# Performance work log

Hardware: AMD Instinct MI355X
Metric: run time of the kernel (lower is better)

## Reference

```python
import jax, jax.numpy as jnp
import numpy as np

B, T, H, W = 2, 16, 16, 16
C_IN, C_ORIG, N_RES, KC, VC = 256, 3, 4, 16, 128
C_ATT = C_IN + C_ORIG          # 259, used for 1/sqrt(c) scale
C_PE = C_ATT + 3               # 262, conv input channels after pos-enc concat
NEG = jnp.float32(-1e30)


def setup_inputs() -> dict:
    key = jax.random.key(0)
    ks = jax.random.split(key, 12)
    f32 = jnp.float32

    def wt(k, shape, fan_in):
        return (jax.random.normal(k, shape, dtype=f32) / np.float32(np.sqrt(fan_in)))

    return {
        "x": jax.random.normal(ks[0], (B, C_IN, T, H, W), dtype=f32),
        "original_input": jax.random.normal(ks[1], (B, C_ORIG, T, H, W), dtype=f32),
        # residual blocks (stacked over N_RES): kernel-2 conv3d, padding 1
        "rb_w1": wt(ks[2], (N_RES, C_IN, C_IN, 2, 2, 2), C_IN * 8),
        "rb_b1": jnp.zeros((N_RES, C_IN), f32),
        "rb_w2": wt(ks[3], (N_RES, 2 * C_IN, C_IN, 2, 2, 2), C_IN * 8),
        "rb_b2": jnp.zeros((N_RES, 2 * C_IN), f32),
        # attention q/k/v 1x1 conv3d == per-pixel linear on 262 channels
        "q_w": wt(ks[4], (KC, C_PE), C_PE), "q_b": jnp.zeros((KC,), f32),
        "k_w": wt(ks[5], (KC, C_PE), C_PE), "k_b": jnp.zeros((KC,), f32),
        "v_w": wt(ks[6], (VC, C_PE), C_PE), "v_b": jnp.zeros((VC,), f32),
        # attention_conv (1x1), res_conv (1x1), out_conv (1x1)
        "attn_w": wt(ks[7], (C_IN, VC), VC), "attn_b": jnp.zeros((C_IN,), f32),
        "resc_w": wt(ks[8], (C_IN, C_IN), C_IN), "resc_b": jnp.zeros((C_IN,), f32),
        "out_w": wt(ks[9], (C_IN, C_IN), C_IN), "out_b": jnp.zeros((C_IN,), f32),
    }


def _conv3d(x, w, b, pad):
    y = jax.lax.conv_general_dilated(
        x, w, window_strides=(1, 1, 1), padding=[(pad, pad)] * 3,
        dimension_numbers=("NCDHW", "OIDHW", "NCDHW"))
    return y + b[None, :, None, None, None]


def _c1(x, w, b):  # 1x1x1 conv
    return jnp.einsum("bcthw,oc->bothw", x, w) + b[None, :, None, None, None]


def _pos_enc(b, t, h, w):
    zt = (-0.5 + jnp.arange(t, dtype=jnp.float32) / t)[None, None, :, None, None]
    zh = (-0.5 + jnp.arange(h, dtype=jnp.float32) / h)[None, None, None, :, None]
    zw = (-0.5 + jnp.arange(w, dtype=jnp.float32) / w)[None, None, None, None, :]
    shp = (b, 1, t, h, w)
    return jnp.concatenate([jnp.broadcast_to(zt, shp),
                            jnp.broadcast_to(zh, shp),
                            jnp.broadcast_to(zw, shp)], axis=1)


def _forward(x, original_input, rb_w1, rb_b1, rb_w2, rb_b2,
             q_w, q_b, k_w, k_b, v_w, v_b,
             attn_w, attn_b, resc_w, resc_b, out_w, out_b):
    b, _, t, h, w = x.shape
    elu = jax.nn.elu

    # --- residual blocks (attention=True variant: k=2 convs, pad=1, crop) ---
    res = x
    for i in range(N_RES):
        o = elu(_conv3d(elu(res), rb_w1[i], rb_b1[i], 1))[:, :, :t, :h, :w]
        o = _conv3d(o, rb_w2[i], rb_b2[i], 1)[:, :, :t, :h, :w]
        c2 = o.shape[1] // 2
        res = res + o[:, :c2] * jax.nn.sigmoid(o[:, c2:])  # gated (identity act)

    # --- attention block on concat(res, original_input) + pos-enc ---
    xa = jnp.concatenate([res, original_input], axis=1)          # (b,259,t,h,w)
    xa = jnp.concatenate([xa, _pos_enc(b, t, h, w)], axis=1)     # (b,262,t,h,w)
    seq = t * h * w
    xf = xa.reshape(b, C_PE, seq).transpose(0, 2, 1)             # (b,seq,262)
    q = xf @ q_w.T + q_b
    k = xf @ k_w.T + k_b
    v = xf @ v_w.T + v_b                                         # (b,seq,VC)

    scores = jnp.einsum("bqc,bkc->bqk", q, k) / np.float32(np.sqrt(C_ATT))
    mask = jnp.tril(jnp.ones((seq, seq), dtype=bool), k=-1)      # mask_center=True
    p = jax.nn.softmax(jnp.where(mask, scores, NEG), axis=-1)
    p = jnp.where(mask, p, 0.0)                                  # row 0 -> zeros
    att = jnp.einsum("bqk,bkc->bqc", p, v)                       # (b,seq,VC)
    att = att.transpose(0, 2, 1).reshape(b, VC, t, h, w)

    att = elu(_c1(elu(att), attn_w, attn_b))
    res = elu(_c1(elu(res), resc_w, resc_b))
    return elu(_c1(elu(res + att), out_w, out_b))


def reference(x, original_input, rb_w1, rb_b1, rb_w2, rb_b2,
              q_w, q_b, k_w, k_b, v_w, v_b,
              attn_w, attn_b, resc_w, resc_b, out_w, out_b):
    return _forward(x, original_input, rb_w1, rb_b1, rb_w2, rb_b2,
                    q_w, q_b, k_w, k_b, v_w, v_b,
                    attn_w, attn_b, resc_w, resc_b, out_w, out_b)
```

## Files before the change

kernel.cpp:

```cpp
#include <hip/hip_runtime.h>
#include <math.h>

#define SEQ 4096
#define CIN 256
#define PROWS 4913
#define PT 289
#define LROW 40
#define NROWS 170
#define GROW 36

typedef __attribute__((ext_vector_type(8))) short bf16x8;
typedef __attribute__((ext_vector_type(4))) float f32x4;

__device__ __forceinline__ float elu_f(float x) {
    return x > 0.0f ? x : (expf(x) - 1.0f);
}
__device__ __forceinline__ unsigned short f2b(float f) {
    unsigned int u = __float_as_uint(f);
    return (unsigned short)((u + 0x7FFFu + ((u >> 16) & 1u)) >> 16);
}

__global__ __launch_bounds__(256) void zero2_kernel(
    uint4* __restrict__ p1, uint4* __restrict__ p2, int n)
{
    int i = blockIdx.x * 256 + threadIdx.x;
    if (i < n) {
        p1[i] = (uint4){0, 0, 0, 0};
        p2[i] = (uint4){0, 0, 0, 0};
    }
}

__global__ __launch_bounds__(256) void prep_t(
    const float* __restrict__ x, unsigned short* __restrict__ elub)
{
    const int b = blockIdx.x >> 5;
    const int s0 = (blockIdx.x & 31) << 7;
    const int cg = blockIdx.y;
    const int tid = threadIdx.x;
    const int s = s0 + (tid & 127);
    const int c0 = cg * 32 + (tid >> 7) * 16;
    const int tt = s >> 8, hh = (s >> 4) & 15, ww = s & 15;
    const size_t prow = (size_t)b * PROWS + (tt + 1) * PT + (hh + 1) * 17 + (ww + 1);
    unsigned short ev[16];
#pragma unroll
    for (int cc = 0; cc < 16; ++cc) {
        float v = x[(((size_t)(b * 256 + c0 + cc)) << 12) + s];
        ev[cc] = f2b(elu_f(v));
    }
    unsigned short* ep = &elub[prow * 256 + c0];
    *(ushort4*)(ep)      = *(ushort4*)&ev[0];
    *(ushort4*)(ep + 4)  = *(ushort4*)&ev[4];
    *(ushort4*)(ep + 8)  = *(ushort4*)&ev[8];
    *(ushort4*)(ep + 12) = *(ushort4*)&ev[12];
}

__global__ __launch_bounds__(256) void wcvt_kernel(
    const float* __restrict__ w1, const float* __restrict__ w2,
    unsigned short* __restrict__ w1t, unsigned short* __restrict__ w2t)
{
    int idx = blockIdx.x * 256 + threadIdx.x;
    if (idx < 2097152) {
        int layer = idx >> 19;
        int rem = idx & 0x7FFFF;
        int frag = rem >> 9;
        int l = (rem >> 3) & 63;
        int e = rem & 7;
        int ks = frag >> 4, mt = frag & 15;
        int tap = ks >> 3, kc = ks & 7;
        int co = mt * 16 + (l & 15);
        int ci = kc * 32 + (l >> 4) * 8 + e;
        w1t[idx] = f2b(w1[(((size_t)(layer * 256 + co)) * 256 + ci) * 8 + tap]);
    }
    if (idx < 4194304) {
        int layer = idx >> 20;
        int rem = idx & 0xFFFFF;
        int frag = rem >> 9;
        int l = (rem >> 3) & 63;
        int e = rem & 7;
        int ks = frag >> 5, mt = frag & 31;
        int tap = ks >> 3, kc = ks & 7;
        int rp = mt * 16 + (l & 15);
        int grp = rp >> 5, sub = rp & 31;
        int co = (sub < 16) ? (grp * 16 + sub) : (256 + grp * 16 + (sub - 16));
        int ci = kc * 32 + (l >> 4) * 8 + e;
        w2t[idx] = f2b(w2[(((size_t)(layer * 512 + co)) * 256 + ci) * 8 + tap]);
    }
}

__global__ __launch_bounds__(256) void conv1_mfma(
    const unsigned short* __restrict__ inP,
    const unsigned short* __restrict__ wfrag,
    const float* __restrict__ bias,
    unsigned short* __restrict__ outP)
{
    __shared__ unsigned short sX[NROWS * LROW];

    const int bx = blockIdx.x;
    const int b = bx >> 6, ptile = bx & 63;
    const int t = ptile >> 2, h0 = (ptile & 3) << 2;
    const int mt0 = blockIdx.y << 2;
    const int tid = threadIdx.x;
    const int lane = tid & 63, wv = tid >> 6;
    const int lr = lane & 15, lg = lane >> 4;

    const unsigned short* inB = inP + (size_t)b * PROWS * 256;

    f32x4 acc[4];
#pragma unroll
    for (int mi = 0; mi < 4; ++mi) acc[mi] = (f32x4){0.f, 0.f, 0.f, 0.f};

    for (int kc = 0; kc < 8; ++kc) {
        const int ci0 = kc << 5;
        __syncthreads();
#pragma unroll
        for (int rnd = 0; rnd < 3; ++rnd) {
            int task = tid + (rnd << 8);
            int row = task >> 2, q = task & 3;
            if (row < NROWS) {
                int dt = row / 85, rem = row - dt * 85;
                int dh = rem / 17, dw = rem - dh * 17;
                int prow = (t + dt) * PT + (h0 + dh) * 17 + dw;
                *(bf16x8*)&sX[row * LROW + (q << 3)] =
                    *(const bf16x8*)(inB + (size_t)prow * 256 + ci0 + (q << 3));
            }
        }
        __syncthreads();
#pragma unroll
        for (int tap = 0; tap < 8; ++tap) {
            const unsigned short* wp = wfrag +
                ((size_t)((((tap << 3) + kc) << 4) + mt0) << 9) + (lane << 3);
            bf16x8 a0 = *(const bf16x8*)(wp);
            bf16x8 a1 = *(const bf16x8*)(wp + 512);
            bf16x8 a2 = *(const bf16x8*)(wp + 1024);
            bf16x8 a3 = *(const bf16x8*)(wp + 1536);
            const int rb = (tap >> 2) * 85 + (wv + ((tap >> 1) & 1)) * 17 + (tap & 1);
            bf16x8 xb = *(const bf16x8*)&sX[(rb + lr) * LROW + (lg << 3)];
            acc[0] = __builtin_amdgcn_mfma_f32_16x16x32_bf16(a0, xb, acc[0], 0, 0, 0);
            acc[1] = __builtin_amdgcn_mfma_f32_16x16x32_bf16(a1, xb, acc[1], 0, 0, 0);
            acc[2] = __builtin_amdgcn_mfma_f32_16x16x32_bf16(a2, xb, acc[2], 0, 0, 0);
            acc[3] = __builtin_amdgcn_mfma_f32_16x16x32_bf16(a3, xb, acc[3], 0, 0, 0);
        }
    }
    const size_t orow = (size_t)b * PROWS + (t + 1) * PT + (h0 + wv + 1) * 17 + (lr + 1);
#pragma unroll
    for (int mi = 0; mi < 4; ++mi) {
        const int cob = ((mt0 + mi) << 4) + (lg << 2);
        unsigned short v4[4];
#pragma unroll
        for (int r = 0; r < 4; ++r)
            v4[r] = f2b(elu_f(acc[mi][r] + bias[cob + r]));
        *(ushort4*)&outP[orow * 256 + cob] = *(ushort4*)v4;
    }
}

__global__ __launch_bounds__(256) void conv2_mfma(
    const unsigned short* __restrict__ inP,
    const unsigned short* __restrict__ wfrag,
    const float* __restrict__ bias,
    float* __restrict__ resf,
    unsigned short* __restrict__ elub)
{
    __shared__ unsigned short sX[NROWS * LROW];

    const int bx = blockIdx.x;
    const int b = bx >> 6, ptile = bx & 63;
    const int t = ptile >> 2, h0 = (ptile & 3) << 2;
    const int mt0 = blockIdx.y << 2;
    const int tid = threadIdx.x;
    const int lane = tid & 63, wv = tid >> 6;
    const int lr = lane & 15, lg = lane >> 4;

    const unsigned short* inB = inP + (size_t)b * PROWS * 256;

    f32x4 acc[4];
#pragma unroll
    for (int mi = 0; mi < 4; ++mi) acc[mi] = (f32x4){0.f, 0.f, 0.f, 0.f};

    for (int kc = 0; kc < 8; ++kc) {
        const int ci0 = kc << 5;
        __syncthreads();
#pragma unroll
        for (int rnd = 0; rnd < 3; ++rnd) {
            int task = tid + (rnd << 8);
            int row = task >> 2, q = task & 3;
            if (row < NROWS) {
                int dt = row / 85, rem = row - dt * 85;
                int dh = rem / 17, dw = rem - dh * 17;
                int prow = (t + dt) * PT + (h0 + dh) * 17 + dw;
                *(bf16x8*)&sX[row * LROW + (q << 3)] =
                    *(const bf16x8*)(inB + (size_t)prow * 256 + ci0 + (q << 3));
            }
        }
        __syncthreads();
#pragma unroll
        for (int tap = 0; tap < 8; ++tap) {
            const unsigned short* wp = wfrag +
                ((size_t)((((tap << 3) + kc) << 5) + mt0) << 9) + (lane << 3);
            bf16x8 a0 = *(const bf16x8*)(wp);
            bf16x8 a1 = *(const bf16x8*)(wp + 512);
            bf16x8 a2 = *(const bf16x8*)(wp + 1024);
            bf16x8 a3 = *(const bf16x8*)(wp + 1536);
            const int rb = (tap >> 2) * 85 + (wv + ((tap >> 1) & 1)) * 17 + (tap & 1);
            bf16x8 xb = *(const bf16x8*)&sX[(rb + lr) * LROW + (lg << 3)];
            acc[0] = __builtin_amdgcn_mfma_f32_16x16x32_bf16(a0, xb, acc[0], 0, 0, 0);
            acc[1] = __builtin_amdgcn_mfma_f32_16x16x32_bf16(a1, xb, acc[1], 0, 0, 0);
            acc[2] = __builtin_amdgcn_mfma_f32_16x16x32_bf16(a2, xb, acc[2], 0, 0, 0);
            acc[3] = __builtin_amdgcn_mfma_f32_16x16x32_bf16(a3, xb, acc[3], 0, 0, 0);
        }
    }
    const int s = (t << 8) + ((h0 + wv) << 4) + lr;
    const size_t prow = (size_t)b * PROWS + (t + 1) * PT + (h0 + wv + 1) * 17 + (lr + 1);
#pragma unroll
    for (int p = 0; p < 2; ++p) {
        const int chb = (((mt0 >> 1) + p) << 4) + (lg << 2);
        unsigned short e4[4];
#pragma unroll
        for (int r = 0; r < 4; ++r) {
            const int ch = chb + r;
            float av = acc[2 * p][r] + bias[ch];
            float gv = acc[2 * p + 1][r] + bias[ch + 256];
            float add = av / (1.0f + expf(-gv));
            size_t ridx = (((size_t)(b * 256 + ch)) << 12) + s;
            float rn = resf[ridx] + add;
            resf[ridx] = rn;
            e4[r] = f2b(elu_f(rn));
        }
        *(ushort4*)&elub[prow * 256 + chb] = *(ushort4*)e4;
    }
}

__global__ __launch_bounds__(256) void pack_kernel(
    const float* __restrict__ res, const float* __restrict__ orig,
    unsigned short* __restrict__ xq)
{
    const int b = blockIdx.x >> 5;
    const int s0 = (blockIdx.x & 31) << 7;
    const int cg = blockIdx.y;
    const int tid = threadIdx.x;
    const int s = s0 + (tid & 127);
    const int c0 = cg * 32 + (tid >> 7) * 16;

    unsigned short xv[16];
    if (cg < 8) {
#pragma unroll
        for (int cc = 0; cc < 16; ++cc) {
            int c = c0 + cc;
            float v = res[(size_t)((b * 256 + c) << 12) + s];
            xv[cc] = f2b(v);
        }
    } else if (cg == 8) {
#pragma unroll
        for (int cc = 0; cc < 16; ++cc) {
            int c = c0 + cc;
            float v;
            if (c < 259)      v = orig[(size_t)((b * 3 + (c - 256)) << 12) + s];
            else if (c == 259) v = -0.5f + (float)(s >> 8) * 0.0625f;
            else if (c == 260) v = -0.5f + (float)((s >> 4) & 15) * 0.0625f;
            else if (c == 261) v = -0.5f + (float)(s & 15) * 0.0625f;
            else               v = 0.0f;
            xv[cc] = f2b(v);
        }
    } else {
#pragma unroll
        for (int cc = 0; cc < 16; ++cc) xv[cc] = 0;
    }
    unsigned short* xp = &xq[((size_t)(b << 12) + s) * 320 + c0];
    *(ushort4*)(xp)      = *(ushort4*)&xv[0];
    *(ushort4*)(xp + 4)  = *(ushort4*)&xv[4];
    *(ushort4*)(xp + 8)  = *(ushort4*)&xv[8];
    *(ushort4*)(xp + 12) = *(ushort4*)&xv[12];
}

__global__ __launch_bounds__(256) void wcvt2_kernel(
    const float* __restrict__ qw, const float* __restrict__ kw,
    const float* __restrict__ vw, const float* __restrict__ aw,
    const float* __restrict__ rw, const float* __restrict__ ow,
    unsigned short* __restrict__ wqkv, unsigned short* __restrict__ awb,
    unsigned short* __restrict__ rwb, unsigned short* __restrict__ owb)
{
    int idx = blockIdx.x * 256 + threadIdx.x;
    if (idx < 61440) {
        int frag = idx >> 9, l = (idx >> 3) & 63, e = idx & 7;
        int kc = frag / 12, mt = frag - kc * 12;
        int r = mt * 16 + (l & 15);
        int c = kc * 32 + ((l >> 4) << 3) + e;
        float v = 0.0f;
        if (c < 262) {
            if (r < 16)       v = qw[r * 262 + c];
            else if (r < 32)  v = kw[(r - 16) * 262 + c];
            else if (r < 160) v = vw[(r - 32) * 262 + c];
        }
        wqkv[idx] = f2b(v);
    } else if (idx < 94208) {
        int j = idx - 61440;
        int frag = j >> 9, l = (j >> 3) & 63, e = j & 7;
        int kc = frag >> 4, mt = frag & 15;
        int r = mt * 16 + (l & 15);
        int c = kc * 32 + ((l >> 4) << 3) + e;
        awb[j] = f2b(aw[r * 128 + c]);
    } else if (idx < 159744) {
        int j = idx - 94208;
        int frag = j >> 9, l = (j >> 3) & 63, e = j & 7;
        int kc = frag >> 4, mt = frag & 15;
        int r = mt * 16 + (l & 15);
        int c = kc * 32 + ((l >> 4) << 3) + e;
        rwb[j] = f2b(rw[r * 256 + c]);
    } else if (idx < 225280) {
        int j = idx - 159744;
        int frag = j >> 9, l = (j >> 3) & 63, e = j & 7;
        int kc = frag >> 4, mt = frag & 15;
        int r = mt * 16 + (l & 15);
        int c = kc * 32 + ((l >> 4) << 3) + e;
        owb[j] = f2b(ow[r * 256 + c]);
    }
}

__global__ __launch_bounds__(256) void qkv_gemm(
    const unsigned short* __restrict__ Wf, const unsigned short* __restrict__ Xt,
    const float* __restrict__ qb, const float* __restrict__ kb,
    const float* __restrict__ vb,
    unsigned short* __restrict__ qbt, unsigned short* __restrict__ kbt,
    unsigned short* __restrict__ vbt)
{
    __shared__ unsigned short sX[128 * GROW];

    const int b = blockIdx.x >> 5;
    const int s0 = (blockIdx.x & 31) << 7;
    const int mt0 = blockIdx.y << 2;
    const int tid = threadIdx.x;
    const int lane = tid & 63, wv = tid >> 6;
    const int lr = lane & 15, lg = lane >> 4;

    f32x4 acc[4][2];
#pragma unroll
    for (int mi = 0; mi < 4; ++mi)
#pragma unroll
        for (int ni = 0; ni < 2; ++ni) acc[mi][ni] = (f32x4){0.f, 0.f, 0.f, 0.f};

    for (int kc = 0; kc < 10; ++kc) {
        __syncthreads();
#pragma unroll
        for (int rnd = 0; rnd < 2; ++rnd) {
            int task = tid + (rnd << 8);
            int row = task >> 2, q = task & 3;
            *(bf16x8*)&sX[row * GROW + (q << 3)] =
                *(const bf16x8*)(Xt + ((size_t)(b << 12) + s0 + row) * 320
                                 + kc * 32 + (q << 3));
        }
        __syncthreads();
        const unsigned short* wp = Wf + ((size_t)(kc * 12 + mt0) << 9) + (lane << 3);
        bf16x8 a0 = *(const bf16x8*)(wp);
        bf16x8 a1 = *(const bf16x8*)(wp + 512);
        bf16x8 a2 = *(const bf16x8*)(wp + 1024);
        bf16x8 a3 = *(const bf16x8*)(wp + 1536);
        bf16x8 x0 = *(const bf16x8*)&sX[(wv * 32 + lr) * GROW + (lg << 3)];
        bf16x8 x1 = *(const bf16x8*)&sX[(wv * 32 + 16 + lr) * GROW + (lg << 3)];
        acc[0][0] = __builtin_amdgcn_mfma_f32_16x16x32_bf16(a0, x0, acc[0][0], 0, 0, 0);
        acc[0][1] = __builtin_amdgcn_mfma_f32_16x16x32_bf16(a0, x1, acc[0][1], 0, 0, 0);
        acc[1][0] = __builtin_amdgcn_mfma_f32_16x16x32_bf16(a1, x0, acc[1][0], 0, 0, 0);
        acc[1][1] = __builtin_amdgcn_mfma_f32_16x16x32_bf16(a1, x1, acc[1][1], 0, 0, 0);
        acc[2][0] = __builtin_amdgcn_mfma_f32_16x16x32_bf16(a2, x0, acc[2][0], 0, 0, 0);
        acc[2][1] = __builtin_amdgcn_mfma_f32_16x16x32_bf16(a2, x1, acc[2][1], 0, 0, 0);
        acc[3][0] = __builtin_amdgcn_mfma_f32_16x16x32_bf16(a3, x0, acc[3][0], 0, 0, 0);
        acc[3][1] = __builtin_amdgcn_mfma_f32_16x16x32_bf16(a3, x1, acc[3][1], 0, 0, 0);
    }
    const int co0 = mt0 << 4;
#pragma unroll
    for (int mi = 0; mi < 4; ++mi)
#pragma unroll
    for (int ni = 0; ni < 2; ++ni)
#pragma unroll
    for (int r = 0; r < 4; ++r) {
        int co = co0 + mi * 16 + lg * 4 + r;
        if (co >= 160) continue;
        int s = s0 + wv * 32 + ni * 16 + lr;
        float bias = (co < 16) ? qb[co] : ((co < 32) ? kb[co - 16] : vb[co - 32]);
        float v = acc[mi][ni][r] + bias;
        if (co < 16)      qbt[((size_t)(b << 12) + s) * 16 + co] = f2b(v);
        else if (co < 32) kbt[((size_t)(b << 12) + s) * 16 + (co - 16)] = f2b(v);
        else              vbt[((size_t)((b << 7) + (co - 32)) << 12) + s] = f2b(v);
    }
}

__global__ __launch_bounds__(256) void attn_part2(
    const unsigned short* __restrict__ qbt, const unsigned short* __restrict__ kbt,
    const unsigned short* __restrict__ vbt,
    float* __restrict__ pacc, float* __restrict__ pml)
{
    const int bx = blockIdx.x;
    const int b = bx >> 8;
    const int qt = (bx >> 2) & 63;
    const int seg = bx & 3;
    const int q0 = qt << 6;
    const int nch = (qt >> 1) + 1;
    const int c_lo = seg << 3;
    if (c_lo >= nch) return;
    const int c_hi = min(c_lo + 8, nch);

    __shared__ unsigned short sK[128 * 16];
    __shared__ unsigned short sP[4][16 * 136];

    const int tid = threadIdx.x;
    const int lane = tid & 63, wv = tid >> 6;
    const int lr = lane & 15, lg = lane >> 4;
    const int qa = q0 + wv * 16 + lr;
    const float scale = 1.0f / sqrtf(259.0f);

    bf16x8 qf = (bf16x8){0, 0, 0, 0, 0, 0, 0, 0};
    if (lg < 2)
        qf = *(const bf16x8*)(qbt + ((size_t)(b << 12) + qa) * 16 + lg * 8);

    f32x4 oacc[8];
#pragma unroll
    for (int vct = 0; vct < 8; ++vct) oacc[vct] = (f32x4){0.f, 0.f, 0.f, 0.f};
    float m = -1e30f, l = 0.0f;

    unsigned short* myP = &sP[wv][0];

    for (int kc = c_lo; kc < c_hi; ++kc) {
        const int kv0 = kc << 7;
        __syncthreads();
        *(bf16x8*)&sK[(tid >> 1) * 16 + (tid & 1) * 8] =
            *(const bf16x8*)(kbt + ((size_t)(b << 12) + kv0 + (tid >> 1)) * 16 + (tid & 1) * 8);
        __syncthreads();

        f32x4 sc[8];
#pragma unroll
        for (int kvt = 0; kvt < 8; ++kvt) {
            bf16x8 af = (bf16x8){0, 0, 0, 0, 0, 0, 0, 0};
            if (lg < 2)
                af = *(const bf16x8*)&sK[(kvt * 16 + lr) * 16 + lg * 8];
            sc[kvt] = __builtin_amdgcn_mfma_f32_16x16x32_bf16(
                af, qf, (f32x4){0.f, 0.f, 0.f, 0.f}, 0, 0, 0);
        }
        float mc = -1e30f;
#pragma unroll
        for (int kvt = 0; kvt < 8; ++kvt) {
#pragma unroll
            for (int r = 0; r < 4; ++r) {
                int kv = kv0 + kvt * 16 + lg * 4 + r;
                float s = (kv < qa) ? sc[kvt][r] * scale : -1e30f;
                sc[kvt][r] = s;
                mc = fmaxf(mc, s);
            }
        }
        mc = fmaxf(mc, __shfl_xor(mc, 16, 64));
        mc = fmaxf(mc, __shfl_xor(mc, 32, 64));
        float mn = fmaxf(m, mc);
        float fac = __expf(m - mn);
        float ls = 0.0f;
#pragma unroll
        for (int kvt = 0; kvt < 8; ++kvt) {
#pragma unroll
            for (int e = 0; e < 2; ++e) {
                float s0v = sc[kvt][2 * e];
                float s1v = sc[kvt][2 * e + 1];
                float p0 = (s0v <= -1e29f) ? 0.f : __expf(s0v - mn);
                float p1 = (s1v <= -1e29f) ? 0.f : __expf(s1v - mn);
                ls += p0 + p1;
                unsigned int pk = (unsigned int)f2b(p0) | ((unsigned int)f2b(p1) << 16);
                int kv = kvt * 16 + lg * 4 + 2 * e;
                *(unsigned int*)&myP[lr * 136 + kv] = pk;
            }
        }
        ls += __shfl_xor(ls, 16, 64);
        ls += __shfl_xor(ls, 32, 64);
        l = l * fac + ls;
        m = mn;
#pragma unroll
        for (int vct = 0; vct < 8; ++vct) {
            oacc[vct][0] *= fac; oacc[vct][1] *= fac;
            oacc[vct][2] *= fac; oacc[vct][3] *= fac;
        }
#pragma unroll
        for (int ks = 0; ks < 4; ++ks) {
            bf16x8 pf = *(const bf16x8*)&myP[lr * 136 + ks * 32 + lg * 8];
#pragma unroll
            for (int vct = 0; vct < 8; ++vct) {
                bf16x8 vf = *(const bf16x8*)(vbt +
                    ((size_t)((b << 7) + vct * 16 + lr) << 12) + kv0 + ks * 32 + lg * 8);
                oacc[vct] = __builtin_amdgcn_mfma_f32_16x16x32_bf16(
                    vf, pf, oacc[vct], 0, 0, 0);
            }
        }
    }

    const int a_ = qt >> 4;
    const int slot = b * 160 + 8 * a_ * (a_ + 1) + (qt & 15) * (a_ + 1) + seg;
    float* ap = pacc + (size_t)slot * 8192;
#pragma unroll
    for (int vct = 0; vct < 8; ++vct)
        *(f32x4*)&ap[(wv * 16 + lr) * 128 + vct * 16 + lg * 4] = oacc[vct];
    if (lg == 0) {
        pml[slot * 128 + (wv * 16 + lr) * 2]     = m;
        pml[slot * 128 + (wv * 16 + lr) * 2 + 1] = l;
    }
}

__global__ __launch_bounds__(256) void attn_combine2(
    const float* __restrict__ pacc, const float* __restrict__ pml,
    unsigned short* __restrict__ attEb)
{
    const int bx = blockIdx.x;
    const int b = bx >> 7;
    const int qt = (bx >> 1) & 63;
    const int half = bx & 1;
    const int a_ = qt >> 4;
    const int nseg_alloc = a_ + 1;
    const int nch = (qt >> 1) + 1;
    const int nseg = (nch + 7) >> 3;
    const int base = b * 160 + 8 * a_ * (a_ + 1) + (qt & 15) * nseg_alloc;
    const int tid = threadIdx.x;
    const int qq = (tid >> 3) + half * 32;
    const int vg = tid & 7;

    float mi_[4], li_[4];
    float m = -1e30f;
    for (int i = 0; i < nseg; ++i) {
        mi_[i] = pml[(base + i) * 128 + qq * 2];
        li_[i] = pml[(base + i) * 128 + qq * 2 + 1];
        m = fmaxf(m, mi_[i]);
    }
    float w[4];
    float l = 0.f;
    for (int i = 0; i < nseg; ++i) {
        float wi = (mi_[i] <= -1e29f) ? 0.f : __expf(mi_[i] - m);
        w[i] = wi;
        l += wi * li_[i];
    }
    float inv = (l > 0.f) ? 1.f / l : 0.f;
    int q = (qt << 6) + qq;
#pragma unroll
    for (int v4 = 0; v4 < 4; ++v4) {
        int vc = vg * 16 + v4 * 4;
        float o0 = 0.f, o1 = 0.f, o2 = 0.f, o3 = 0.f;
        for (int i = 0; i < nseg; ++i) {
            f32x4 a = *(const f32x4*)(pacc + (size_t)(base + i) * 8192 + qq * 128 + vc);
            o0 = fmaf(w[i], a[0], o0);
            o1 = fmaf(w[i], a[1], o1);
            o2 = fmaf(w[i], a[2], o2);
            o3 = fmaf(w[i], a[3], o3);
        }
        unsigned short r0 = f2b(elu_f(o0 * inv));
        unsigned short r1 = f2b(elu_f(o1 * inv));
        unsigned short r2 = f2b(elu_f(o2 * inv));
        unsigned short r3 = f2b(elu_f(o3 * inv));
        ushort4 pk = {r0, r1, r2, r3};
        *(ushort4*)&attEb[((size_t)(b << 12) + q) * 128 + vc] = pk;
    }
}

__global__ __launch_bounds__(256) void final_ab_gemm(
    const unsigned short* __restrict__ W1f, const unsigned short* __restrict__ W2f,
    const unsigned short* __restrict__ X1, const unsigned short* __restrict__ X2,
    const float* __restrict__ b1, const float* __restrict__ b2,
    unsigned short* __restrict__ sum2b)
{
    __shared__ unsigned short sX[128 * GROW];

    const int b = blockIdx.x >> 5;
    const int s0 = (blockIdx.x & 31) << 7;
    const int mt0 = blockIdx.y << 2;
    const int tid = threadIdx.x;
    const int lane = tid & 63, wv = tid >> 6;
    const int lr = lane & 15, lg = lane >> 4;

    f32x4 acc1[4][2], acc2[4][2];
#pragma unroll
    for (int mi = 0; mi < 4; ++mi)
#pragma unroll
        for (int ni = 0; ni < 2; ++ni) {
            acc1[mi][ni] = (f32x4){0.f, 0.f, 0.f, 0.f};
            acc2[mi][ni] = (f32x4){0.f, 0.f, 0.f, 0.f};
        }

    for (int kc = 0; kc < 4; ++kc) {
        __syncthreads();
#pragma unroll
        for (int rnd = 0; rnd < 2; ++rnd) {
            int task = tid + (rnd << 8);
            int row = task >> 2, q = task & 3;
            *(bf16x8*)&sX[row * GROW + (q << 3)] =
                *(const bf16x8*)(X1 + ((size_t)(b << 12) + s0 + row) * 128
                                 + kc * 32 + (q << 3));
        }
        __syncthreads();
        const unsigned short* wp = W1f + ((size_t)((kc << 4) + mt0) << 9) + (lane << 3);
        bf16x8 a0 = *(const bf16x8*)(wp);
        bf16x8 a1 = *(const bf16x8*)(wp + 512);
        bf16x8 a2 = *(const bf16x8*)(wp + 1024);
        bf16x8 a3 = *(const bf16x8*)(wp + 1536);
        bf16x8 x0 = *(const bf16x8*)&sX[(wv * 32 + lr) * GROW + (lg << 3)];
        bf16x8 x1 = *(const bf16x8*)&sX[(wv * 32 + 16 + lr) * GROW + (lg << 3)];
        acc1[0][0] = __builtin_amdgcn_mfma_f32_16x16x32_bf16(a0, x0, acc1[0][0], 0, 0, 0);
        acc1[0][1] = __builtin_amdgcn_mfma_f32_16x16x32_bf16(a0, x1, acc1[0][1], 0, 0, 0);
        acc1[1][0] = __builtin_amdgcn_mfma_f32_16x16x32_bf16(a1, x0, acc1[1][0], 0, 0, 0);
        acc1[1][1] = __builtin_amdgcn_mfma_f32_16x16x32_bf16(a1, x1, acc1[1][1], 0, 0, 0);
        acc1[2][0] = __builtin_amdgcn_mfma_f32_16x16x32_bf16(a2, x0, acc1[2][0], 0, 0, 0);
        acc1[2][1] = __builtin_amdgcn_mfma_f32_16x16x32_bf16(a2, x1, acc1[2][1], 0, 0, 0);
        acc1[3][0] = __builtin_amdgcn_mfma_f32_16x16x32_bf16(a3, x0, acc1[3][0], 0, 0, 0);
        acc1[3][1] = __builtin_amdgcn_mfma_f32_16x16x32_bf16(a3, x1, acc1[3][1], 0, 0, 0);
    }
    for (int kc = 0; kc < 8; ++kc) {
        __syncthreads();
#pragma unroll
        for (int rnd = 0; rnd < 2; ++rnd) {
            int task = tid + (rnd << 8);
            int row = task >> 2, q = task & 3;
            int s = s0 + row;
            int tt = s >> 8, hh = (s >> 4) & 15, ww = s & 15;
            size_t prow = (size_t)b * PROWS + (tt + 1) * PT + (hh + 1) * 17 + (ww + 1);
            *(bf16x8*)&sX[row * GROW + (q << 3)] =
                *(const bf16x8*)(X2 + prow * 256 + kc * 32 + (q << 3));
        }
        __syncthreads();
        const unsigned short* wp = W2f + ((size_t)((kc << 4) + mt0) << 9) + (lane << 3);
        bf16x8 a0 = *(const bf16x8*)(wp);
        bf16x8 a1 = *(const bf16x8*)(wp + 512);
        bf16x8 a2 = *(const bf16x8*)(wp + 1024);
        bf16x8 a3 = *(const bf16x8*)(wp + 1536);
        bf16x8 x0 = *(const bf16x8*)&sX[(wv * 32 + lr) * GROW + (lg << 3)];
        bf16x8 x1 = *(const bf16x8*)&sX[(wv * 32 + 16 + lr) * GROW + (lg << 3)];
        acc2[0][0] = __builtin_amdgcn_mfma_f32_16x16x32_bf16(a0, x0, acc2[0][0], 0, 0, 0);
        acc2[0][1] = __builtin_amdgcn_mfma_f32_16x16x32_bf16(a0, x1, acc2[0][1], 0, 0, 0);
        acc2[1][0] = __builtin_amdgcn_mfma_f32_16x16x32_bf16(a1, x0, acc2[1][0], 0, 0, 0);
        acc2[1][1] = __builtin_amdgcn_mfma_f32_16x16x32_bf16(a1, x1, acc2[1][1], 0, 0, 0);
        acc2[2][0] = __builtin_amdgcn_mfma_f32_16x16x32_bf16(a2, x0, acc2[2][0], 0, 0, 0);
        acc2[2][1] = __builtin_amdgcn_mfma_f32_16x16x32_bf16(a2, x1, acc2[2][1], 0, 0, 0);
        acc2[3][0] = __builtin_amdgcn_mfma_f32_16x16x32_bf16(a3, x0, acc2[3][0], 0, 0, 0);
        acc2[3][1] = __builtin_amdgcn_mfma_f32_16x16x32_bf16(a3, x1, acc2[3][1], 0, 0, 0);
    }
    const int co0 = mt0 << 4;
#pragma unroll
    for (int mi = 0; mi < 4; ++mi)
#pragma unroll
    for (int ni = 0; ni < 2; ++ni)
#pragma unroll
    for (int r = 0; r < 4; ++r) {
        int co = co0 + mi * 16 + lg * 4 + r;
        int s = s0 + wv * 32 + ni * 16 + lr;
        float v1 = elu_f(acc1[mi][ni][r] + b1[co]);
        float v2 = elu_f(acc2[mi][ni][r] + b2[co]);
        sum2b[((size_t)(b << 12) + s) * 256 + co] = f2b(elu_f(v1 + v2));
    }
}

__global__ __launch_bounds__(256) void final_c_gemm(
    const unsigned short* __restrict__ Wf, const unsigned short* __restrict__ Xt,
    const float* __restrict__ bias, float* __restrict__ out)
{
    __shared__ unsigned short sX[128 * GROW];

    const int b = blockIdx.x >> 5;
    const int s0 = (blockIdx.x & 31) << 7;
    const int mt0 = blockIdx.y << 2;
    const int tid = threadIdx.x;
    const int lane = tid & 63, wv = tid >> 6;
    const int lr = lane & 15, lg = lane >> 4;

    f32x4 acc[4][2];
#pragma unroll
    for (int mi = 0; mi < 4; ++mi)
#pragma unroll
        for (int ni = 0; ni < 2; ++ni) acc[mi][ni] = (f32x4){0.f, 0.f, 0.f, 0.f};

    for (int kc = 0; kc < 8; ++kc) {
        __syncthreads();
#pragma unroll
        for (int rnd = 0; rnd < 2; ++rnd) {
            int task = tid + (rnd << 8);
            int row = task >> 2, q = task & 3;
            *(bf16x8*)&sX[row * GROW + (q << 3)] =
                *(const bf16x8*)(Xt + ((size_t)(b << 12) + s0 + row) * 256
                                 + kc * 32 + (q << 3));
        }
        __syncthreads();
        const unsigned short* wp = Wf + ((size_t)((kc << 4) + mt0) << 9) + (lane << 3);
        bf16x8 a0 = *(const bf16x8*)(wp);
        bf16x8 a1 = *(const bf16x8*)(wp + 512);
        bf16x8 a2 = *(const bf16x8*)(wp + 1024);
        bf16x8 a3 = *(const bf16x8*)(wp + 1536);
        bf16x8 x0 = *(const bf16x8*)&sX[(wv * 32 + lr) * GROW + (lg << 3)];
        bf16x8 x1 = *(const bf16x8*)&sX[(wv * 32 + 16 + lr) * GROW + (lg << 3)];
        acc[0][0] = __builtin_amdgcn_mfma_f32_16x16x32_bf16(a0, x0, acc[0][0], 0, 0, 0);
        acc[0][1] = __builtin_amdgcn_mfma_f32_16x16x32_bf16(a0, x1, acc[0][1], 0, 0, 0);
        acc[1][0] = __builtin_amdgcn_mfma_f32_16x16x32_bf16(a1, x0, acc[1][0], 0, 0, 0);
        acc[1][1] = __builtin_amdgcn_mfma_f32_16x16x32_bf16(a1, x1, acc[1][1], 0, 0, 0);
        acc[2][0] = __builtin_amdgcn_mfma_f32_16x16x32_bf16(a2, x0, acc[2][0], 0, 0, 0);
        acc[2][1] = __builtin_amdgcn_mfma_f32_16x16x32_bf16(a2, x1, acc[2][1], 0, 0, 0);
        acc[3][0] = __builtin_amdgcn_mfma_f32_16x16x32_bf16(a3, x0, acc[3][0], 0, 0, 0);
        acc[3][1] = __builtin_amdgcn_mfma_f32_16x16x32_bf16(a3, x1, acc[3][1], 0, 0, 0);
    }
    const int co0 = mt0 << 4;
#pragma unroll
    for (int mi = 0; mi < 4; ++mi)
#pragma unroll
    for (int ni = 0; ni < 2; ++ni)
#pragma unroll
    for (int r = 0; r < 4; ++r) {
        int co = co0 + mi * 16 + lg * 4 + r;
        int s = s0 + wv * 32 + ni * 16 + lr;
        out[((size_t)(b * 256 + co) << 12) + s] = elu_f(acc[mi][ni][r] + bias[co]);
    }
}

extern "C" void kernel_launch(void* const* d_in, const int* in_sizes, int n_in,
                              void* d_out, int out_size, void* d_ws, size_t ws_size,
                              hipStream_t stream) {
    const float* x      = (const float*)d_in[0];
    const float* orig   = (const float*)d_in[1];
    const float* rb_w1  = (const float*)d_in[2];
    const float* rb_b1  = (const float*)d_in[3];
    const float* rb_w2  = (const float*)d_in[4];
    const float* rb_b2  = (const float*)d_in[5];
    const float* q_w    = (const float*)d_in[6];
    const float* q_b    = (const float*)d_in[7];
    const float* k_w    = (const float*)d_in[8];
    const float* k_b    = (const float*)d_in[9];
    const float* v_w    = (const float*)d_in[10];
    const float* v_b    = (const float*)d_in[11];
    const float* attn_w = (const float*)d_in[12];
    const float* attn_b = (const float*)d_in[13];
    const float* resc_w = (const float*)d_in[14];
    const float* resc_b = (const float*)d_in[15];
    const float* out_w  = (const float*)d_in[16];
    const float* out_b  = (const float*)d_in[17];
    float* out = (float*)d_out;

    char* base = (char*)d_ws;
    float*          res   = (float*)(base);
    unsigned short* elubP = (unsigned short*)(base + (8u << 20));
    unsigned short* o1P   = (unsigned short*)(base + (13u << 20));
    unsigned short* w1t   = (unsigned short*)(base + (18u << 20));
    unsigned short* w2t   = (unsigned short*)(base + (22u << 20));
    unsigned short* vbt   = o1P;
    unsigned short* attEb = (unsigned short*)(base + (15u << 20));
    unsigned short* sum2b = w1t;
    unsigned short* xqkvB = w2t;
    float*          pacc  = (float*)(base + (22u << 20));
    unsigned short* qbt   = (unsigned short*)(base + (32u << 20));
    unsigned short* kbt   = (unsigned short*)(base + (32u << 20) + 262144);
    unsigned short* wqkvB = (unsigned short*)(base + (32u << 20) + 524288);
    unsigned short* attnWb= (unsigned short*)(base + (32u << 20) + 655360);
    unsigned short* rescWb= (unsigned short*)(base + (32u << 20) + 720896);
    unsigned short* outWb = (unsigned short*)(base + (32u << 20) + 851968);
    float*          pml   = (float*)(base + (32u << 20) + 983040);

    const int nz = (2 * PROWS * 256 * 2) / 16;
    zero2_kernel<<<(nz + 255) / 256, 256, 0, stream>>>(
        (uint4*)elubP, (uint4*)o1P, nz);

    hipMemcpyAsync(res, x, (size_t)2097152 * sizeof(float),
                   hipMemcpyDeviceToDevice, stream);
    prep_t<<<dim3(64, 8), 256, 0, stream>>>(x, elubP);
    wcvt_kernel<<<16384, 256, 0, stream>>>(rb_w1, rb_w2, w1t, w2t);

    for (int i = 0; i < 4; ++i) {
        conv1_mfma<<<dim3(128, 4), 256, 0, stream>>>(
            elubP, w1t + (size_t)i * 524288, rb_b1 + i * 256, o1P);
        conv2_mfma<<<dim3(128, 8), 256, 0, stream>>>(
            o1P, w2t + (size_t)i * 1048576, rb_b2 + i * 512, res, elubP);
    }

    pack_kernel<<<dim3(64, 10), 256, 0, stream>>>(res, orig, xqkvB);
    wcvt2_kernel<<<880, 256, 0, stream>>>(q_w, k_w, v_w, attn_w, resc_w, out_w,
                                          wqkvB, attnWb, rescWb, outWb);

    qkv_gemm<<<dim3(64, 3), 256, 0, stream>>>(wqkvB, xqkvB, q_b, k_b, v_b,
                                              qbt, kbt, vbt);

    attn_part2<<<512, 256, 0, stream>>>(qbt, kbt, vbt, pacc, pml);
    attn_combine2<<<256, 256, 0, stream>>>(pacc, pml, attEb);

    final_ab_gemm<<<dim3(64, 4), 256, 0, stream>>>(
        attnWb, rescWb, attEb, elubP, attn_b, resc_b, sum2b);

    final_c_gemm<<<dim3(64, 4), 256, 0, stream>>>(outWb, sum2b, out_b, out);
}
```

Baseline: 420.6 us.

## Stage 64-channel K chunks in LDS and widen conv2 output tile

Both residual conv kernels now load 64 input channels per shared-memory stage instead of 32, with a wider padded row stride. This halves the number of barrier and load rounds per block. conv2 also gives each block 8 output M-tiles instead of 4 and launches half as many blocks, so every staged input tile is reused across twice as many output channels. In exchange, conv2 holds more accumulator registers and uses more LDS per block, and the smaller grid lowers parallelism, which may reduce occupancy.

Result: slower. 929.3 us (+121.0%).

```diff
diff --git a/kernel.cpp b/kernel.cpp
--- a/kernel.cpp
+++ b/kernel.cpp
@@ -5,7 +5,7 @@
 #define CIN 256
 #define PROWS 4913
 #define PT 289
-#define LROW 40
+#define LROW2 72
 #define NROWS 170
 #define GROW 36
 
@@ -93,7 +93,7 @@
     const float* __restrict__ bias,
     unsigned short* __restrict__ outP)
 {
-    __shared__ unsigned short sX[NROWS * LROW];
+    __shared__ unsigned short sX[NROWS * LROW2];
 
     const int bx = blockIdx.x;
     const int b = bx >> 6, ptile = bx & 63;
@@ -109,36 +109,40 @@
 #pragma unroll
     for (int mi = 0; mi < 4; ++mi) acc[mi] = (f32x4){0.f, 0.f, 0.f, 0.f};
 
-    for (int kc = 0; kc < 8; ++kc) {
-        const int ci0 = kc << 5;
-        __syncthreads();
-#pragma unroll
-        for (int rnd = 0; rnd < 3; ++rnd) {
+    for (int kcp = 0; kcp < 4; ++kcp) {
+        const int ci0 = kcp << 6;
+        __syncthreads();
+#pragma unroll
+        for (int rnd = 0; rnd < 6; ++rnd) {
             int task = tid + (rnd << 8);
-            int row = task >> 2, q = task & 3;
+            int row = task >> 3, q = task & 7;
             if (row < NROWS) {
                 int dt = row / 85, rem = row - dt * 85;
                 int dh = rem / 17, dw = rem - dh * 17;
                 int prow = (t + dt) * PT + (h0 + dh) * 17 + dw;
-                *(bf16x8*)&sX[row * LROW + (q << 3)] =
+                *(bf16x8*)&sX[row * LROW2 + (q << 3)] =
                     *(const bf16x8*)(inB + (size_t)prow * 256 + ci0 + (q << 3));
             }
         }
         __syncthreads();
 #pragma unroll
         for (int tap = 0; tap < 8; ++tap) {
-            const unsigned short* wp = wfrag +
-                ((size_t)((((tap << 3) + kc) << 4) + mt0) << 9) + (lane << 3);
-            bf16x8 a0 = *(const bf16x8*)(wp);
-            bf16x8 a1 = *(const bf16x8*)(wp + 512);
-            bf16x8 a2 = *(const bf16x8*)(wp + 1024);
-            bf16x8 a3 = *(const bf16x8*)(wp + 1536);
             const int rb = (tap >> 2) * 85 + (wv + ((tap >> 1) & 1)) * 17 + (tap & 1);
-            bf16x8 xb = *(const bf16x8*)&sX[(rb + lr) * LROW + (lg << 3)];
-            acc[0] = __builtin_amdgcn_mfma_f32_16x16x32_bf16(a0, xb, acc[0], 0, 0, 0);
-            acc[1] = __builtin_amdgcn_mfma_f32_16x16x32_bf16(a1, xb, acc[1], 0, 0, 0);
-            acc[2] = __builtin_amdgcn_mfma_f32_16x16x32_bf16(a2, xb, acc[2], 0, 0, 0);
-            acc[3] = __builtin_amdgcn_mfma_f32_16x16x32_bf16(a3, xb, acc[3], 0, 0, 0);
+#pragma unroll
+            for (int g = 0; g < 2; ++g) {
+                const int kc = (kcp << 1) + g;
+                const unsigned short* wp = wfrag +
+                    ((size_t)((((tap << 3) + kc) << 4) + mt0) << 9) + (lane << 3);
+                bf16x8 a0 = *(const bf16x8*)(wp);
+                bf16x8 a1 = *(const bf16x8*)(wp + 512);
+                bf16x8 a2 = *(const bf16x8*)(wp + 1024);
+                bf16x8 a3 = *(const bf16x8*)(wp + 1536);
+                bf16x8 xb = *(const bf16x8*)&sX[(rb + lr) * LROW2 + (g << 5) + (lg << 3)];
+                acc[0] = __builtin_amdgcn_mfma_f32_16x16x32_bf16(a0, xb, acc[0], 0, 0, 0);
+                acc[1] = __builtin_amdgcn_mfma_f32_16x16x32_bf16(a1, xb, acc[1], 0, 0, 0);
+                acc[2] = __builtin_amdgcn_mfma_f32_16x16x32_bf16(a2, xb, acc[2], 0, 0, 0);
+                acc[3] = __builtin_amdgcn_mfma_f32_16x16x32_bf16(a3, xb, acc[3], 0, 0, 0);
+            }
         }
     }
     const size_t orow = (size_t)b * PROWS + (t + 1) * PT + (h0 + wv + 1) * 17 + (lr + 1);
@@ -160,58 +164,59 @@
     float* __restrict__ resf,
     unsigned short* __restrict__ elub)
 {
-    __shared__ unsigned short sX[NROWS * LROW];
+    __shared__ unsigned short sX[NROWS * LROW2];
 
     const int bx = blockIdx.x;
     const int b = bx >> 6, ptile = bx & 63;
     const int t = ptile >> 2, h0 = (ptile & 3) << 2;
-    const int mt0 = blockIdx.y << 2;
+    const int mt0 = blockIdx.y << 3;
     const int tid = threadIdx.x;
     const int lane = tid & 63, wv = tid >> 6;
     const int lr = lane & 15, lg = lane >> 4;
 
     const unsigned short* inB = inP + (size_t)b * PROWS * 256;
 
-    f32x4 acc[4];
-#pragma unroll
-    for (int mi = 0; mi < 4; ++mi) acc[mi] = (f32x4){0.f, 0.f, 0.f, 0.f};
-
-    for (int kc = 0; kc < 8; ++kc) {
-        const int ci0 = kc << 5;
-        __syncthreads();
-#pragma unroll
-        for (int rnd = 0; rnd < 3; ++rnd) {
+    f32x4 acc[8];
+#pragma unroll
+    for (int mi = 0; mi < 8; ++mi) acc[mi] = (f32x4){0.f, 0.f, 0.f, 0.f};
+
+    for (int kcp = 0; kcp < 4; ++kcp) {
+        const int ci0 = kcp << 6;
+        __syncthreads();
+#pragma unroll
+        for (int rnd = 0; rnd < 6; ++rnd) {
             int task = tid + (rnd << 8);
-            int row = task >> 2, q = task & 3;
+            int row = task >> 3, q = task & 7;
             if (row < NROWS) {
                 int dt = row / 85, rem = row - dt * 85;
                 int dh = rem / 17, dw = rem - dh * 17;
                 int prow = (t + dt) * PT + (h0 + dh) * 17 + dw;
-                *(bf16x8*)&sX[row * LROW + (q << 3)] =
+                *(bf16x8*)&sX[row * LROW2 + (q << 3)] =
                     *(const bf16x8*)(inB + (size_t)prow * 256 + ci0 + (q << 3));
             }
         }
         __syncthreads();
 #pragma unroll
         for (int tap = 0; tap < 8; ++tap) {
-            const unsigned short* wp = wfrag +
-                ((size_t)((((tap << 3) + kc) << 5) + mt0) << 9) + (lane << 3);
-            bf16x8 a0 = *(const bf16x8*)(wp);
-            bf16x8 a1 = *(const bf16x8*)(wp + 512);
-            bf16x8 a2 = *(const bf16x8*)(wp + 1024);
-            bf16x8 a3 = *(const bf16x8*)(wp + 1536);
             const int rb = (tap >> 2) * 85 + (wv + ((tap >> 1) & 1)) * 17 + (tap & 1);
-            bf16x8 xb = *(const bf16x8*)&sX[(rb + lr) * LROW + (lg << 3)];
-            acc[0] = __builtin_amdgcn_mfma_f32_16x16x32_bf16(a0, xb, acc[0], 0, 0, 0);
-            acc[1] = __builtin_amdgcn_mfma_f32_16x16x32_bf16(a1, xb, acc[1], 0, 0, 0);
-            acc[2] = __builtin_amdgcn_mfma_f32_16x16x32_bf16(a2, xb, acc[2], 0, 0, 0);
-            acc[3] = __builtin_amdgcn_mfma_f32_16x16x32_bf16(a3, xb, acc[3], 0, 0, 0);
+#pragma unroll
+            for (int g = 0; g < 2; ++g) {
+                const int kc = (kcp << 1) + g;
+                const unsigned short* wp = wfrag +
+                    ((size_t)((((tap << 3) + kc) << 5) + mt0) << 9) + (lane << 3);
+                bf16x8 xb = *(const bf16x8*)&sX[(rb + lr) * LROW2 + (g << 5) + (lg << 3)];
+#pragma unroll
+                for (int mi = 0; mi < 8; ++mi) {
+                    bf16x8 am = *(const bf16x8*)(wp + (mi << 9));
+                    acc[mi] = __builtin_amdgcn_mfma_f32_16x16x32_bf16(am, xb, acc[mi], 0, 0, 0);
+                }
+            }
         }
     }
     const int s = (t << 8) + ((h0 + wv) << 4) + lr;
     const size_t prow = (size_t)b * PROWS + (t + 1) * PT + (h0 + wv + 1) * 17 + (lr + 1);
 #pragma unroll
-    for (int p = 0; p < 2; ++p) {
+    for (int p = 0; p < 4; ++p) {
         const int chb = (((mt0 >> 1) + p) << 4) + (lg << 2);
         unsigned short e4[4];
 #pragma unroll
@@ -758,7 +763,7 @@
     for (int i = 0; i < 4; ++i) {
         conv1_mfma<<<dim3(128, 4), 256, 0, stream>>>(
             elubP, w1t + (size_t)i * 524288, rb_b1 + i * 256, o1P);
-        conv2_mfma<<<dim3(128, 8), 256, 0, stream>>>(
+        conv2_mfma<<<dim3(128, 4), 256, 0, stream>>>(
             o1P, w2t + (size_t)i * 1048576, rb_b2 + i * 512, res, elubP);
     }
 
```
